# Performance work log

Measured on AMD Instinct MI355X. Metric: run time of the kernel, lower is better.

## Reference

```python
import jax, jax.numpy as jnp
import numpy as np

NUM_HEADS = 8
NUM_GROUPS = 32
EPS = 1e-5


def setup_inputs() -> dict:
    key = jax.random.key(0)
    ks = jax.random.split(key, 7)
    B, C, H, W = 16, 512, 32, 32
    x = jax.random.normal(ks[0], (B, C, H, W), dtype=jnp.float32)
    gn_gamma = jnp.ones((C,), dtype=jnp.float32)
    gn_beta = jnp.zeros((C,), dtype=jnp.float32)
    # Conv1d with kernel_size=1 is a per-position matmul: weight [out, in]
    qkv_w = jax.random.normal(ks[1], (3 * C, C), dtype=jnp.float32) / np.sqrt(C)
    qkv_b = jax.random.normal(ks[2], (3 * C,), dtype=jnp.float32) * 0.01
    proj_w = jax.random.normal(ks[3], (C, C), dtype=jnp.float32) / np.sqrt(C)
    proj_b = jax.random.normal(ks[4], (C,), dtype=jnp.float32) * 0.01
    return {"x": x, "gn_gamma": gn_gamma, "gn_beta": gn_beta,
            "qkv_w": qkv_w, "qkv_b": qkv_b, "proj_w": proj_w, "proj_b": proj_b}


def group_norm(x, gamma, beta):
    # x: [B, C, H, W]
    B, C, H, W = x.shape
    xg = x.reshape(B, NUM_GROUPS, C // NUM_GROUPS, H, W)
    mean = xg.mean(axis=(2, 3, 4), keepdims=True)
    var = xg.var(axis=(2, 3, 4), keepdims=True)
    xg = (xg - mean) * jax.lax.rsqrt(var + EPS)
    x = xg.reshape(B, C, H, W)
    return x * gamma[None, :, None, None] + beta[None, :, None, None]


def reference(x, gn_gamma, gn_beta, qkv_w, qkv_b, proj_w, proj_b):
    B, C, H, W = x.shape
    N = H * W
    hd = C // NUM_HEADS  # head dim
    h = group_norm(x, gn_gamma, gn_beta).reshape(B, C, N)
    # 1x1 Conv1d == matmul over channel dim
    qkv = jnp.einsum('oc,bcn->bon', qkv_w, h) + qkv_b[None, :, None]
    qkv = qkv.reshape(B, 3, NUM_HEADS, hd, N)
    q, k, v = qkv[:, 0], qkv[:, 1], qkv[:, 2]  # each [B, h, d, N]
    scale = hd ** (-0.5)
    attn = jnp.einsum('bhdn,bhdm->bhnm', q, k) * scale  # [B, h, N, N]
    attn = jax.nn.softmax(attn, axis=-1)
    out = jnp.einsum('bhnm,bhdm->bhdn', attn, v).reshape(B, C, N)
    out = jnp.einsum('oc,bcn->bon', proj_w, out) + proj_b[None, :, None]
    return x + out.reshape(B, C, H, W)
```

## Files before the change

### kernel.cpp

```cpp
#include <hip/hip_runtime.h>

typedef unsigned short u16;
typedef unsigned int u32;
typedef __bf16 bf16x8 __attribute__((ext_vector_type(8)));
typedef float f32x4 __attribute__((ext_vector_type(4)));
typedef float f32x16 __attribute__((ext_vector_type(16)));

#define B_ 16
#define C_ 512
#define N_ 1024
#define NB_ 16384
#define K_ 512
#define M3_ 1536
#define SCALE_Q 0.18033688011112042f

__device__ __forceinline__ u16 f2bf(float f) {
  u32 u = __float_as_uint(f);
  u32 r = (u + 0x7FFFu + ((u >> 16) & 1u)) >> 16;
  return (u16)r;
}

__device__ __forceinline__ void gl_lds16(const void* g, void* l) {
  __builtin_amdgcn_global_load_lds(
      (const __attribute__((address_space(1))) u32*)(uintptr_t)g,
      (__attribute__((address_space(3))) u32*)(u32)(uintptr_t)l, 16, 0, 0);
}

__device__ __forceinline__ u32 cvtpk(float lo, float hi) {
  u32 r;
  asm("v_cvt_pk_bf16_f32 %0, %1, %2" : "=v"(r) : "v"(lo), "v"(hi));
  return r;
}

__device__ __forceinline__ float exp2a(float x) {
  float r;
  asm("v_exp_f32 %0, %1" : "=v"(r) : "v"(x));
  return r;
}

__device__ __forceinline__ void plswap2(u32& a, u32& b) {
#if __has_builtin(__builtin_amdgcn_permlane32_swap)
  auto r = __builtin_amdgcn_permlane32_swap((int)a, (int)b, false, false);
  a = (u32)r[0];
  b = (u32)r[1];
#else
  asm("v_permlane32_swap_b32 %0, %1" : "+v"(a), "+v"(b));
#endif
}

__device__ __forceinline__ float xhalf_sum(float x) {
  u32 a = __float_as_uint(x), b = a;
  plswap2(a, b);
  return __uint_as_float(a) + __uint_as_float(b);
}

__global__ __launch_bounds__(256) void cast_bf16_kernel(const float* __restrict__ src,
                                                        u16* __restrict__ dst, int n) {
  int i = blockIdx.x * 256 + threadIdx.x;
  if (i < n) dst[i] = f2bf(src[i]);
}

__global__ __launch_bounds__(256) void gnorm_kernel(const float* __restrict__ x,
                                                    const float* __restrict__ gamma,
                                                    const float* __restrict__ beta,
                                                    u16* __restrict__ ht) {
  int blk = blockIdx.x;
  int b = blk >> 5, g = blk & 31;
  int t = threadIdx.x;
  const float* xb = x + ((size_t)(b * C_ + g * 16) << 10);
  float v[16][4];
  float s = 0.f, sq = 0.f;
#pragma unroll
  for (int cc = 0; cc < 16; ++cc) {
#pragma unroll
    for (int r = 0; r < 4; ++r) {
      float f = xb[cc * 1024 + r * 256 + t];
      v[cc][r] = f; s += f; sq += f * f;
    }
  }
#pragma unroll
  for (int m = 32; m >= 1; m >>= 1) { s += __shfl_xor(s, m, 64); sq += __shfl_xor(sq, m, 64); }
  __shared__ float red[8];
  int w = t >> 6;
  if ((t & 63) == 0) { red[w * 2] = s; red[w * 2 + 1] = sq; }
  __syncthreads();
  s = red[0] + red[2] + red[4] + red[6];
  sq = red[1] + red[3] + red[5] + red[7];
  float mean = s * (1.f / 16384.f);
  float var = sq * (1.f / 16384.f) - mean * mean;
  float rstd = rsqrtf(var + 1e-5f);
  float gm[16], bt[16];
#pragma unroll
  for (int cc = 0; cc < 16; ++cc) {
    gm[cc] = gamma[g * 16 + cc] * rstd;
    bt[cc] = beta[g * 16 + cc];
  }
  u16* hb = ht + ((size_t)(b << 10)) * C_ + g * 16;
#pragma unroll
  for (int r = 0; r < 4; ++r) {
    u32 pk[8];
#pragma unroll
    for (int q = 0; q < 8; ++q) {
      float f0 = (v[2 * q][r] - mean) * gm[2 * q] + bt[2 * q];
      float f1 = (v[2 * q + 1][r] - mean) * gm[2 * q + 1] + bt[2 * q + 1];
      pk[q] = (u32)f2bf(f0) | ((u32)f2bf(f1) << 16);
    }
    u16* dp = hb + (size_t)(r * 256 + t) * C_;
    uint4 a = {pk[0], pk[1], pk[2], pk[3]};
    uint4 b4 = {pk[4], pk[5], pk[6], pk[7]};
    *(uint4*)dp = a;
    *(uint4*)(dp + 8) = b4;
  }
}

template <int EPI>
__global__ __launch_bounds__(256) void gemm_kernel(const u16* __restrict__ A,
                                                   const u16* __restrict__ BT,
                                                   const float* __restrict__ bias,
                                                   u16* __restrict__ Co,
                                                   u16* __restrict__ qTo,
                                                   u16* __restrict__ kTo,
                                                   const float* __restrict__ xres,
                                                   float* __restrict__ Fo) {
  __shared__ u16 ldsA[128 * 64];
  __shared__ u16 ldsB[128 * 64];
  int t = threadIdx.x;
  int l = t & 63, w = t >> 6;
  int wr = w >> 1, wc = w & 1;
  int ro0 = blockIdx.y * 128, co0 = blockIdx.x * 128;
  f32x4 acc[4][4];
#pragma unroll
  for (int m = 0; m < 4; ++m)
#pragma unroll
    for (int n = 0; n < 4; ++n) acc[m][n] = {0.f, 0.f, 0.f, 0.f};
  int srow = t >> 3, sg = t & 7;
  for (int kt = 0; kt < 8; ++kt) {
    int k0 = kt * 64;
#pragma unroll
    for (int i = 0; i < 4; ++i) {
      int row = i * 32 + srow;
      int gl = sg ^ (row & 7);
      gl_lds16(A + (size_t)(ro0 + row) * K_ + k0 + gl * 8, ldsA + (i * 32 + w * 8) * 64);
      gl_lds16(BT + (size_t)(co0 + row) * K_ + k0 + gl * 8, ldsB + (i * 32 + w * 8) * 64);
    }
    __syncthreads();
#pragma unroll
    for (int ks = 0; ks < 2; ++ks) {
      bf16x8 af[4], bfr[4];
#pragma unroll
      for (int m = 0; m < 4; ++m) {
        int row = wr * 64 + m * 16 + (l & 15);
        int ph = (ks * 4 + (l >> 4)) ^ (row & 7);
        af[m] = *(const bf16x8*)&ldsA[row * 64 + ph * 8];
      }
#pragma unroll
      for (int n = 0; n < 4; ++n) {
        int row = wc * 64 + n * 16 + (l & 15);
        int ph = (ks * 4 + (l >> 4)) ^ (row & 7);
        bfr[n] = *(const bf16x8*)&ldsB[row * 64 + ph * 8];
      }
#pragma unroll
      for (int m = 0; m < 4; ++m)
#pragma unroll
        for (int n = 0; n < 4; ++n)
          acc[m][n] = __builtin_amdgcn_mfma_f32_16x16x32_bf16(af[m], bfr[n], acc[m][n], 0, 0, 0);
    }
    __syncthreads();
  }
  if (EPI == 0 && ro0 < 1024) {
    int sel = ro0 >> 9;
    u16* dstb = sel ? kTo : qTo;
    float scl = sel ? 1.f : SCALE_Q;
#pragma unroll
    for (int m = 0; m < 4; ++m) {
      int row0 = ro0 + wr * 64 + m * 16 + (l >> 4) * 4;
      int o = row0 & 511;
      int h = o >> 6, d0 = o & 63;
      float bv0 = bias[row0], bv1 = bias[row0 + 1];
      float bv2 = bias[row0 + 2], bv3 = bias[row0 + 3];
#pragma unroll
      for (int n = 0; n < 4; ++n) {
        int col = co0 + wc * 64 + n * 16 + (l & 15);
        int bb = col >> 10, nn = col & 1023;
        float v0 = (acc[m][n][0] + bv0) * scl;
        float v1 = (acc[m][n][1] + bv1) * scl;
        float v2 = (acc[m][n][2] + bv2) * scl;
        float v3 = (acc[m][n][3] + bv3) * scl;
        uint2 ov = {cvtpk(v0, v1), cvtpk(v2, v3)};
        *(uint2*)(dstb + ((size_t)((bb * 8 + h) << 10) + nn) * 64 + d0) = ov;
      }
    }
  } else {
#pragma unroll
    for (int m = 0; m < 4; ++m) {
#pragma unroll
      for (int j = 0; j < 4; ++j) {
        int row = ro0 + wr * 64 + m * 16 + (l >> 4) * 4 + j;
        float bv = bias[row];
#pragma unroll
        for (int n = 0; n < 4; ++n) {
          int col = co0 + wc * 64 + n * 16 + (l & 15);
          float val = acc[m][n][j] + bv;
          if (EPI == 0) {
            Co[(size_t)row * NB_ + col] = f2bf(val);
          } else {
            int bb = col >> 10, nn = col & 1023;
            size_t oi = (((size_t)(bb * C_ + row)) << 10) + nn;
            Fo[oi] = xres[oi] + val;
          }
        }
      }
    }
  }
}

__global__ __launch_bounds__(256) void attn_kernel(const u16* __restrict__ qT,
                                                   const u16* __restrict__ kT,
                                                   const u16* __restrict__ qkv,
                                                   u16* __restrict__ aoT) {
  __shared__ u16 KV[2][4096];
  int bid = blockIdx.x;
  int wid = (bid & 7) * 128 + (bid >> 3);
  int qt2 = wid & 7, h = (wid >> 3) & 7, b = wid >> 6;
  int bh = b * 8 + h;
  int t = threadIdx.x, l = t & 63, w = t >> 6;
  int lq = l & 31, hi = l >> 5;
  int q0 = qt2 * 128 + w * 32;

  const u16* qbase = qT + ((size_t)(bh << 10) + q0 + lq) * 64 + hi * 8;
  bf16x8 qf[4];
#pragma unroll
  for (int kc = 0; kc < 4; ++kc) qf[kc] = *(const bf16x8*)(qbase + kc * 16);

  f32x16 accO[2];
#pragma unroll
  for (int dt = 0; dt < 2; ++dt)
#pragma unroll
    for (int r = 0; r < 16; ++r) accO[dt][r] = 0.f;
  float lsum = 0.f;

  const u16 *src0, *src1;
  u32 ldso0, ldso1;
  int adv;
  if (w < 2) {
    int i0 = 2 * w, i1 = 2 * w + 1;
    src0 = kT + ((size_t)(bh << 10) + i0 * 8 + (l >> 3)) * 64 + (((l & 7) ^ ((l >> 3) & 7)) * 8);
    src1 = kT + ((size_t)(bh << 10) + i1 * 8 + (l >> 3)) * 64 + (((l & 7) ^ ((l >> 3) & 7)) * 8);
    ldso0 = i0 * 512; ldso1 = i1 * 512;
    adv = 2048;
  } else {
    int j0 = 2 * (w - 2), j1 = 2 * (w - 2) + 1;
    src0 = qkv + (size_t)(2 * C_ + h * 64 + j0 * 16 + (l >> 2)) * NB_ + (b << 10) +
           (((l & 3) ^ ((l >> 3) & 3)) * 8);
    src1 = qkv + (size_t)(2 * C_ + h * 64 + j1 * 16 + (l >> 2)) * NB_ + (b << 10) +
           (((l & 3) ^ ((l >> 3) & 3)) * 8);
    ldso0 = 2048 + j0 * 512; ldso1 = 2048 + j1 * 512;
    adv = 32;
  }

  const u16* kfp[4];
#pragma unroll
  for (int kc = 0; kc < 4; ++kc)
    kfp[kc] = &KV[0][0] + lq * 64 + (((2 * kc + hi) ^ (lq & 7)) * 8);
  const u16* vfp[4];
#pragma unroll
  for (int dt = 0; dt < 2; ++dt)
#pragma unroll
    for (int kcc = 0; kcc < 2; ++kcc)
      vfp[dt * 2 + kcc] = &KV[0][0] + 2048 + (dt * 32 + lq) * 32 +
                          (((kcc * 2 + hi) ^ ((lq >> 1) & 3)) * 8);

  auto stage = [&](int buf) {
    gl_lds16(src0, &KV[buf][0] + ldso0);
    gl_lds16(src1, &KV[buf][0] + ldso1);
    src0 += adv;
    src1 += adv;
  };

  auto step = [&](int buf, bool dostage) {
    asm volatile("s_waitcnt vmcnt(0)" ::: "memory");
    __builtin_amdgcn_sched_barrier(0);
    __builtin_amdgcn_s_barrier();
    __builtin_amdgcn_sched_barrier(0);
    if (dostage) stage(buf ^ 1);
    bf16x8 kf[4];
#pragma unroll
    for (int kc = 0; kc < 4; ++kc) kf[kc] = *(const bf16x8*)(kfp[kc] + buf * 4096);
    f32x16 sc;
#pragma unroll
    for (int r = 0; r < 16; ++r) sc[r] = 0.f;
    __builtin_amdgcn_s_setprio(1);
#pragma unroll
    for (int kc = 0; kc < 4; ++kc)
      sc = __builtin_amdgcn_mfma_f32_32x32x16_bf16(kf[kc], qf[kc], sc, 0, 0, 0);
    __builtin_amdgcn_s_setprio(0);
    bf16x8 vf[4];
#pragma unroll
    for (int j = 0; j < 4; ++j) vf[j] = *(const bf16x8*)(vfp[j] + buf * 4096);
    float p0 = 0.f, p1 = 0.f, p2 = 0.f, p3 = 0.f;
#pragma unroll
    for (int r = 0; r < 4; ++r) {
      float e0 = exp2a(sc[4 * r + 0]);
      float e1 = exp2a(sc[4 * r + 1]);
      float e2 = exp2a(sc[4 * r + 2]);
      float e3 = exp2a(sc[4 * r + 3]);
      sc[4 * r + 0] = e0; sc[4 * r + 1] = e1;
      sc[4 * r + 2] = e2; sc[4 * r + 3] = e3;
      p0 += e0; p1 += e1; p2 += e2; p3 += e3;
    }
    lsum += (p0 + p1) + (p2 + p3);
    u32 pk[8];
#pragma unroll
    for (int p = 0; p < 8; ++p) pk[p] = cvtpk(sc[2 * p], sc[2 * p + 1]);
    u32 pfu[2][4];
#pragma unroll
    for (int cc = 0; cc < 2; ++cc) {
      u32 w0 = pk[cc * 4 + 0], w2 = pk[cc * 4 + 2];
      u32 w1 = pk[cc * 4 + 1], w3 = pk[cc * 4 + 3];
      plswap2(w0, w2);
      plswap2(w1, w3);
      pfu[cc][0] = w0; pfu[cc][1] = w1; pfu[cc][2] = w2; pfu[cc][3] = w3;
    }
    __builtin_amdgcn_s_setprio(1);
#pragma unroll
    for (int kcc = 0; kcc < 2; ++kcc)
#pragma unroll
      for (int dt = 0; dt < 2; ++dt) {
        union { u32 u[4]; bf16x8 v; } pf;
        pf.u[0] = pfu[kcc][0]; pf.u[1] = pfu[kcc][1];
        pf.u[2] = pfu[kcc][2]; pf.u[3] = pfu[kcc][3];
        accO[dt] = __builtin_amdgcn_mfma_f32_32x32x16_bf16(vf[dt * 2 + kcc], pf.v, accO[dt], 0, 0, 0);
      }
    __builtin_amdgcn_s_setprio(0);
  };

  stage(0);
#pragma unroll 1
  for (int s = 0; s < 15; ++s) {
    step(0, true);
    step(1, true);
  }
  step(0, true);
  step(1, false);

  float inv = 1.0f / xhalf_sum(lsum);
  u16* ob = aoT + ((size_t)((b << 10) + q0 + lq)) * C_ + h * 64;
#pragma unroll
  for (int dt = 0; dt < 2; ++dt)
#pragma unroll
    for (int rg = 0; rg < 4; ++rg) {
      int d0 = dt * 32 + rg * 8 + hi * 4;
      u32 w0 = cvtpk(accO[dt][rg * 4 + 0] * inv, accO[dt][rg * 4 + 1] * inv);
      u32 w1 = cvtpk(accO[dt][rg * 4 + 2] * inv, accO[dt][rg * 4 + 3] * inv);
      uint2 o = {w0, w1};
      *(uint2*)(ob + d0) = o;
    }
}

extern "C" void kernel_launch(void* const* d_in, const int* in_sizes, int n_in,
                              void* d_out, int out_size, void* d_ws, size_t ws_size,
                              hipStream_t stream) {
  const float* x = (const float*)d_in[0];
  const float* gamma = (const float*)d_in[1];
  const float* beta = (const float*)d_in[2];
  const float* qkv_w = (const float*)d_in[3];
  const float* qkv_b = (const float*)d_in[4];
  const float* proj_w = (const float*)d_in[5];
  const float* proj_b = (const float*)d_in[6];
  float* out = (float*)d_out;
  char* ws = (char*)d_ws;
  u16* wq = (u16*)(ws);
  u16* wp = (u16*)(ws + 1572864);
  u16* ht = (u16*)(ws + 2097152);
  u16* qkvo = (u16*)(ws + 18874368);
  u16* qT = (u16*)(ws + 69206016);
  u16* kT = (u16*)(ws + 85983232);
  u16* aoT = ht;

  cast_bf16_kernel<<<3072, 256, 0, stream>>>(qkv_w, wq, M3_ * K_);
  cast_bf16_kernel<<<1024, 256, 0, stream>>>(proj_w, wp, C_ * K_);
  gnorm_kernel<<<512, 256, 0, stream>>>(x, gamma, beta, ht);
  gemm_kernel<0><<<dim3(128, 12), 256, 0, stream>>>(wq, ht, qkv_b, qkvo, qT, kT, nullptr, nullptr);
  attn_kernel<<<1024, 256, 0, stream>>>(qT, kT, qkvo, aoT);
  gemm_kernel<1><<<dim3(128, 4), 256, 0, stream>>>(wp, aoT, proj_b, nullptr, nullptr, nullptr, x, out);
}
```

Before: 131.3 us.

## Triple-buffer attention KV with software-pipelined QK, merge casts, remap GEMM blocks per XCD

The attention loop moves to a three-buffer LDS ring and computes the QK^T MFMA for the next tile before the softmax and PV of the current tile. This overlaps the score MFMAs with the exp and PV work and lets loads run further ahead. The two weight-cast launches are merged into one kernel to save a launch. GEMM block indices are remapped so neighbouring column tiles land on the same XCD, aiming at better L2 reuse. The cost is more LDS per block and a second live score accumulator, which may lower occupancy.

```diff
diff --git a/kernel.cpp b/kernel.cpp
--- a/kernel.cpp
+++ b/kernel.cpp
@@ -54,10 +54,18 @@
   return __uint_as_float(a) + __uint_as_float(b);
 }
 
-__global__ __launch_bounds__(256) void cast_bf16_kernel(const float* __restrict__ src,
-                                                        u16* __restrict__ dst, int n) {
+__global__ __launch_bounds__(256) void cast2_kernel(const float* __restrict__ a,
+                                                    const float* __restrict__ b,
+                                                    u16* __restrict__ da,
+                                                    u16* __restrict__ db,
+                                                    int na, int nb) {
   int i = blockIdx.x * 256 + threadIdx.x;
-  if (i < n) dst[i] = f2bf(src[i]);
+  if (i < na) {
+    da[i] = f2bf(a[i]);
+  } else {
+    int j = i - na;
+    if (j < nb) db[j] = f2bf(b[j]);
+  }
 }
 
 __global__ __launch_bounds__(256) void gnorm_kernel(const float* __restrict__ x,
@@ -127,7 +135,11 @@
   int t = threadIdx.x;
   int l = t & 63, w = t >> 6;
   int wr = w >> 1, wc = w & 1;
-  int ro0 = blockIdx.y * 128, co0 = blockIdx.x * 128;
+  int lid = blockIdx.y * 128 + blockIdx.x;
+  int xcd = lid & 7, j2 = lid >> 3;
+  int bx = xcd * 16 + (j2 & 15);
+  int by = j2 >> 4;
+  int ro0 = by * 128, co0 = bx * 128;
   f32x4 acc[4][4];
 #pragma unroll
   for (int m = 0; m < 4; ++m)
@@ -218,7 +230,7 @@
                                                    const u16* __restrict__ kT,
                                                    const u16* __restrict__ qkv,
                                                    u16* __restrict__ aoT) {
-  __shared__ u16 KV[2][4096];
+  __shared__ u16 KV[3][4096];
   int bid = blockIdx.x;
   int wid = (bid & 7) * 128 + (bid >> 3);
   int qt2 = wid & 7, h = (wid >> 3) & 7, b = wid >> 6;
@@ -258,35 +270,27 @@
     adv = 32;
   }
 
-  const u16* kfp[4];
+  u32 kfo[4], vfo[4];
 #pragma unroll
   for (int kc = 0; kc < 4; ++kc)
-    kfp[kc] = &KV[0][0] + lq * 64 + (((2 * kc + hi) ^ (lq & 7)) * 8);
-  const u16* vfp[4];
+    kfo[kc] = lq * 64 + (((2 * kc + hi) ^ (lq & 7)) * 8);
 #pragma unroll
   for (int dt = 0; dt < 2; ++dt)
 #pragma unroll
     for (int kcc = 0; kcc < 2; ++kcc)
-      vfp[dt * 2 + kcc] = &KV[0][0] + 2048 + (dt * 32 + lq) * 32 +
-                          (((kcc * 2 + hi) ^ ((lq >> 1) & 3)) * 8);
-
-  auto stage = [&](int buf) {
-    gl_lds16(src0, &KV[buf][0] + ldso0);
-    gl_lds16(src1, &KV[buf][0] + ldso1);
+      vfo[dt * 2 + kcc] = 2048 + (dt * 32 + lq) * 32 + (((kcc * 2 + hi) ^ ((lq >> 1) & 3)) * 8);
+
+  auto stageTo = [&](u16* buf) {
+    gl_lds16(src0, buf + ldso0);
+    gl_lds16(src1, buf + ldso1);
     src0 += adv;
     src1 += adv;
   };
 
-  auto step = [&](int buf, bool dostage) {
-    asm volatile("s_waitcnt vmcnt(0)" ::: "memory");
-    __builtin_amdgcn_sched_barrier(0);
-    __builtin_amdgcn_s_barrier();
-    __builtin_amdgcn_sched_barrier(0);
-    if (dostage) stage(buf ^ 1);
+  auto qk = [&](const u16* buf, f32x16& sc) {
     bf16x8 kf[4];
 #pragma unroll
-    for (int kc = 0; kc < 4; ++kc) kf[kc] = *(const bf16x8*)(kfp[kc] + buf * 4096);
-    f32x16 sc;
+    for (int kc = 0; kc < 4; ++kc) kf[kc] = *(const bf16x8*)(buf + kfo[kc]);
 #pragma unroll
     for (int r = 0; r < 16; ++r) sc[r] = 0.f;
     __builtin_amdgcn_s_setprio(1);
@@ -294,9 +298,12 @@
     for (int kc = 0; kc < 4; ++kc)
       sc = __builtin_amdgcn_mfma_f32_32x32x16_bf16(kf[kc], qf[kc], sc, 0, 0, 0);
     __builtin_amdgcn_s_setprio(0);
+  };
+
+  auto finish = [&](const u16* buf, f32x16& sc) {
     bf16x8 vf[4];
 #pragma unroll
-    for (int j = 0; j < 4; ++j) vf[j] = *(const bf16x8*)(vfp[j] + buf * 4096);
+    for (int j = 0; j < 4; ++j) vf[j] = *(const bf16x8*)(buf + vfo[j]);
     float p0 = 0.f, p1 = 0.f, p2 = 0.f, p3 = 0.f;
 #pragma unroll
     for (int r = 0; r < 4; ++r) {
@@ -334,14 +341,41 @@
     __builtin_amdgcn_s_setprio(0);
   };
 
-  stage(0);
+#define WAITBAR(N)                                       \
+  asm volatile("s_waitcnt vmcnt(" #N ")" ::: "memory"); \
+  __builtin_amdgcn_sched_barrier(0);                     \
+  __builtin_amdgcn_s_barrier();                          \
+  __builtin_amdgcn_sched_barrier(0);
+
+  u16* pa = &KV[0][0];
+  u16* pb = &KV[1][0];
+  u16* pc = &KV[2][0];
+  f32x16 scA, scB;
+
+  stageTo(pa);
+  stageTo(pb);
+  WAITBAR(0)
+  qk(pa, scA);
+
 #pragma unroll 1
   for (int s = 0; s < 15; ++s) {
-    step(0, true);
-    step(1, true);
-  }
-  step(0, true);
-  step(1, false);
+    WAITBAR(0)
+    stageTo(pc);
+    qk(pb, scB);
+    finish(pa, scA);
+    u16* tp = pa; pa = pb; pb = pc; pc = tp;
+    WAITBAR(0)
+    stageTo(pc);
+    qk(pb, scA);
+    finish(pa, scB);
+    tp = pa; pa = pb; pb = pc; pc = tp;
+  }
+  WAITBAR(0)
+  qk(pb, scB);
+  finish(pa, scA);
+  pa = pb;
+  finish(pa, scB);
+#undef WAITBAR
 
   float inv = 1.0f / xhalf_sum(lsum);
   u16* ob = aoT + ((size_t)((b << 10) + q0 + lq)) * C_ + h * 64;
@@ -377,8 +411,7 @@
   u16* kT = (u16*)(ws + 85983232);
   u16* aoT = ht;
 
-  cast_bf16_kernel<<<3072, 256, 0, stream>>>(qkv_w, wq, M3_ * K_);
-  cast_bf16_kernel<<<1024, 256, 0, stream>>>(proj_w, wp, C_ * K_);
+  cast2_kernel<<<4096, 256, 0, stream>>>(qkv_w, proj_w, wq, wp, M3_ * K_, C_ * K_);
   gnorm_kernel<<<512, 256, 0, stream>>>(x, gamma, beta, ht);
   gemm_kernel<0><<<dim3(128, 12), 256, 0, stream>>>(wq, ht, qkv_b, qkvo, qT, kT, nullptr, nullptr);
   attn_kernel<<<1024, 256, 0, stream>>>(qT, kT, qkvo, aoT);
```

New measurement: 128.8 us. No clear change (-1.9%).
